# Kernel tuning notes

Hardware: AMD Instinct MI355X
Metric: run time of the kernel (lower is better)

## Reference

```python
import jax, jax.numpy as jnp
import numpy as np

D = 768
B, T = 4, 4096


def _layernorm(x, gamma, bias):
    # Faithful to the (buggy) original: (x - mu/sqrt(var)) * gamma + bias,
    # with torch's default unbiased variance (ddof=1).
    mu = jnp.mean(x, axis=-1, keepdims=True)
    var = jnp.var(x, axis=-1, keepdims=True, ddof=1)
    return (x - mu / jnp.sqrt(var)) * gamma + bias


def setup_inputs() -> dict:
    key = jax.random.key(0)
    ks = jax.random.split(key, 8)
    # kaiming_uniform_ default: bound = sqrt(6 / fan_in) with a=sqrt(5) -> gain = sqrt(2/(1+5)) = sqrt(1/3)
    # bound = gain * sqrt(3/fan_in) = sqrt(1/fan_in)
    bound_attn = 1.0 / np.sqrt(D)
    bound_lin = 1.0 / np.sqrt(D)  # torch Linear default init bound
    return {
        "x": jax.random.normal(ks[0], (B, T, D), dtype=jnp.float32),
        "ln1_g": jnp.ones((D,), jnp.float32),
        "ln1_b": jnp.zeros((D,), jnp.float32),
        "wq": jax.random.uniform(ks[1], (D, D), jnp.float32, -bound_attn, bound_attn),
        "wk": jax.random.uniform(ks[2], (D, D), jnp.float32, -bound_attn, bound_attn),
        "wv": jax.random.uniform(ks[3], (D, D), jnp.float32, -bound_attn, bound_attn),
        "ln2_g": jnp.ones((D,), jnp.float32),
        "ln2_b": jnp.zeros((D,), jnp.float32),
        "fc1_w": jax.random.uniform(ks[4], (D, D), jnp.float32, -bound_lin, bound_lin),
        "fc1_b": jax.random.uniform(ks[5], (D,), jnp.float32, -bound_lin, bound_lin),
        "fc2_w": jax.random.uniform(ks[6], (D, D), jnp.float32, -bound_lin, bound_lin),
        "fc2_b": jax.random.uniform(ks[7], (D,), jnp.float32, -bound_lin, bound_lin),
    }


def reference(x, ln1_g, ln1_b, wq, wk, wv, ln2_g, ln2_b, fc1_w, fc1_b, fc2_w, fc2_b):
    d_model = x.shape[-1]
    # LN 1
    y = _layernorm(x, ln1_g, ln1_b)
    # Naive single-head attention (no causal mask, scale 1/sqrt(d_model))
    q = jnp.einsum("btk,kd->btd", y, wq)
    k = jnp.einsum("btk,kd->btd", y, wk)
    v = jnp.einsum("btk,kd->btd", y, wv)
    scale = 1.0 / jnp.sqrt(jnp.asarray(d_model, y.dtype))
    a = jax.nn.softmax(jnp.einsum("bqd,bkd->bqk", q, k) * scale, axis=-1)
    y = jnp.einsum("bqt,btd->bqd", a, v)
    # LN 2
    y = _layernorm(y, ln2_g, ln2_b)
    # MLP: Linear -> ReLU -> Linear (Dropout in eval mode = identity)
    h = jax.nn.relu(jnp.einsum("btd,od->bto", y, fc1_w) + fc1_b)
    y = jnp.einsum("btd,od->bto", h, fc2_w) + fc2_b
    # Residual
    return x + y
```

## Files before the change

### kernel.cpp

```cpp
#include <hip/hip_runtime.h>
#include <hip/hip_bf16.h>


#define DDIM 768
#define TT   4096
#define NB   4
#define ROWS (NB * TT)

using bf16 = __hip_bfloat16;
typedef __bf16 bf16x8 __attribute__((ext_vector_type(8)));
typedef float  f32x4  __attribute__((ext_vector_type(4)));
typedef unsigned short us4 __attribute__((ext_vector_type(4)));

__device__ __forceinline__ float to_f(float x) { return x; }
__device__ __forceinline__ float to_f(bf16 x) { return __bfloat162float(x); }

__device__ __forceinline__ unsigned short bfb(float f) {
  bf16 b = __float2bfloat16(f);
  return __builtin_bit_cast(unsigned short, b);
}

__device__ __forceinline__ void gload16(const void* g, void* l) {
#if __has_builtin(__builtin_amdgcn_global_load_lds)
  __builtin_amdgcn_global_load_lds(
      (const __attribute__((address_space(1))) void*)g,
      (__attribute__((address_space(3))) void*)l, 16, 0, 0);
#else
  int lane = threadIdx.x & 63;
  ((int4*)l)[lane] = *(const int4*)g;
#endif
}

template <int MODE, int SWZ, int NT, int MT>
__global__ __launch_bounds__(256) void gemm_bt(
    const bf16* __restrict__ A, int lda, long sA,
    const bf16* __restrict__ B, int ldb, long sB,
    void* __restrict__ Cout, int ldc, long sC, int K, float scale,
    const float* __restrict__ bias, const float* __restrict__ resid,
    float* __restrict__ Lsum) {
  __shared__ __align__(16) bf16 As[128 * 32];
  __shared__ __align__(16) bf16 Bs[128 * 32];
  __shared__ float Lred[128];

  int bx, by, bz;
  if constexpr (SWZ == 1) {
    const int h   = blockIdx.x;
    const int xcd = h & 7;
    const int s   = h >> 3;
    bx = s % NT;
    const int g = (s / NT) * 8 + xcd;
    by = g % MT;
    bz = g / MT;
  } else if constexpr (SWZ == 2) {
    const int h   = blockIdx.x;
    const int xcd = h & 7;
    const int s   = h >> 3;
    by = s % MT;
    const int g = (s / MT) * 8 + xcd;
    bx = g % NT;
    bz = g / NT;
  } else {
    bx = blockIdx.x; by = blockIdx.y; bz = blockIdx.z;
  }

  A += (long)bz * sA;
  B += (long)bz * sB;

  const int tid  = threadIdx.x;
  const int wave = tid >> 6;
  const int lane = tid & 63;
  const int l16  = lane & 15;
  const int lq   = lane >> 4;
  const int wm   = wave >> 1;
  const int wn   = wave & 1;
  const long tileM = (long)by * 128;
  const long tileN = (long)bx * 128;

  if constexpr (MODE == 5) {
    if (tid < 128) Lred[tid] = 0.f;
  }

  f32x4 acc[4][4] = {};

  const int c0 = wave * 128 + lane;
  const int c1 = c0 + 64;
  bf16* ldsA0 = &As[(wave * 128 + 0) * 8];
  bf16* ldsA1 = &As[(wave * 128 + 64) * 8];
  bf16* ldsB0 = &Bs[(wave * 128 + 0) * 8];
  bf16* ldsB1 = &Bs[(wave * 128 + 64) * 8];
  const long ar0 = (tileM + (c0 >> 2)) * (long)lda + (c0 & 3) * 8;
  const long ar1 = (tileM + (c1 >> 2)) * (long)lda + (c1 & 3) * 8;
  const long br0 = (tileN + (c0 >> 2)) * (long)ldb + (c0 & 3) * 8;
  const long br1 = (tileN + (c1 >> 2)) * (long)ldb + (c1 & 3) * 8;

  for (int k0 = 0; k0 < K; k0 += 32) {
    gload16(A + ar0 + k0, ldsA0);
    gload16(A + ar1 + k0, ldsA1);
    gload16(B + br0 + k0, ldsB0);
    gload16(B + br1 + k0, ldsB1);
    __syncthreads();

    bf16x8 af[4], bf_[4];
#pragma unroll
    for (int i = 0; i < 4; ++i)
      af[i] = *(const bf16x8*)&As[(wm * 64 + i * 16 + l16) * 32 + lq * 8];
#pragma unroll
    for (int j = 0; j < 4; ++j)
      bf_[j] = *(const bf16x8*)&Bs[(wn * 64 + j * 16 + l16) * 32 + lq * 8];
#pragma unroll
    for (int i = 0; i < 4; ++i)
#pragma unroll
      for (int j = 0; j < 4; ++j)
        acc[i][j] = __builtin_amdgcn_mfma_f32_16x16x32_bf16(af[i], bf_[j],
                                                            acc[i][j], 0, 0, 0);
    __syncthreads();
  }

  const long base_m = tileM + wm * 64;
  const long base_n = tileN + wn * 64;

  if constexpr (MODE == 5) {
    bf16* P = (bf16*)Cout + (long)bz * sC;
    float ps[4] = {0.f, 0.f, 0.f, 0.f};
#pragma unroll
    for (int j = 0; j < 4; ++j) {
      const long colq = base_n + j * 16 + l16;
#pragma unroll
      for (int i = 0; i < 4; ++i) {
        const long krow = base_m + i * 16 + lq * 4;
        const float p0 = exp2f(acc[i][j][0] * scale);
        const float p1 = exp2f(acc[i][j][1] * scale);
        const float p2 = exp2f(acc[i][j][2] * scale);
        const float p3 = exp2f(acc[i][j][3] * scale);
        ps[j] += (p0 + p1) + (p2 + p3);
        us4 w = {bfb(p0), bfb(p1), bfb(p2), bfb(p3)};
        *(us4*)(P + colq * (long)ldc + krow) = w;
      }
    }
#pragma unroll
    for (int j = 0; j < 4; ++j) {
      float v = ps[j];
      v += __shfl_xor(v, 16);
      v += __shfl_xor(v, 32);
      if (lq == 0) atomicAdd(&Lred[wn * 64 + j * 16 + l16], v);
    }
    __syncthreads();
    if (tid < 128) atomicAdd(&Lsum[(long)bz * TT + tileN + tid], Lred[tid]);
  } else if constexpr (MODE == 6) {
    bf16* Op = (bf16*)Cout + (long)bz * sC;
    float inv[4];
#pragma unroll
    for (int j = 0; j < 4; ++j)
      inv[j] = 1.0f / Lsum[(long)bz * TT + base_n + j * 16 + l16];
#pragma unroll
    for (int j = 0; j < 4; ++j) {
      const long colq = base_n + j * 16 + l16;
#pragma unroll
      for (int i = 0; i < 4; ++i) {
        const long drow = base_m + i * 16 + lq * 4;
        us4 w = {bfb(acc[i][j][0] * inv[j]), bfb(acc[i][j][1] * inv[j]),
                 bfb(acc[i][j][2] * inv[j]), bfb(acc[i][j][3] * inv[j])};
        *(us4*)(Op + colq * (long)ldc + drow) = w;
      }
    }
  } else if constexpr (MODE == 3) {
    bf16* Hp = (bf16*)Cout;
#pragma unroll
    for (int i = 0; i < 4; ++i) {
      const long drow = base_m + i * 16 + lq * 4;
      const f32x4 bv = *(const f32x4*)&bias[drow];
#pragma unroll
      for (int j = 0; j < 4; ++j) {
        const long colt = base_n + j * 16 + l16;
        float v0 = acc[i][j][0] + bv[0]; v0 = v0 > 0.f ? v0 : 0.f;
        float v1 = acc[i][j][1] + bv[1]; v1 = v1 > 0.f ? v1 : 0.f;
        float v2 = acc[i][j][2] + bv[2]; v2 = v2 > 0.f ? v2 : 0.f;
        float v3 = acc[i][j][3] + bv[3]; v3 = v3 > 0.f ? v3 : 0.f;
        us4 w = {bfb(v0), bfb(v1), bfb(v2), bfb(v3)};
        *(us4*)(Hp + colt * (long)ldc + drow) = w;
      }
    }
  } else {
    float* Op = (float*)Cout;
#pragma unroll
    for (int i = 0; i < 4; ++i) {
      const long drow = base_m + i * 16 + lq * 4;
      const f32x4 bv = *(const f32x4*)&bias[drow];
#pragma unroll
      for (int j = 0; j < 4; ++j) {
        const long off = (base_n + j * 16 + l16) * (long)ldc + drow;
        const f32x4 rs = *(const f32x4*)&resid[off];
        f32x4 o;
        o[0] = acc[i][j][0] + bv[0] + rs[0];
        o[1] = acc[i][j][1] + bv[1] + rs[1];
        o[2] = acc[i][j][2] + bv[2] + rs[2];
        o[3] = acc[i][j][3] + bv[3] + rs[3];
        __builtin_nontemporal_store(o, (f32x4*)(Op + off));
      }
    }
  }
}

__global__ __launch_bounds__(256) void gemm_qkv(
    const bf16* __restrict__ Y,
    const bf16* __restrict__ Wq, const bf16* __restrict__ Wk,
    const bf16* __restrict__ Wv, bf16* __restrict__ Qm,
    bf16* __restrict__ Km, bf16* __restrict__ Vt) {
  __shared__ __align__(16) bf16 As[128 * 32];
  __shared__ __align__(16) bf16 Bs[128 * 32];

  const int z = blockIdx.z;
  const bf16* Ap = (z == 2) ? Wv : Y;
  const bf16* Bp = (z == 0) ? Wq : (z == 1) ? Wk : Y;

  const int tid  = threadIdx.x;
  const int wave = tid >> 6;
  const int lane = tid & 63;
  const int l16  = lane & 15;
  const int lq   = lane >> 4;
  const int wm   = wave >> 1;
  const int wn   = wave & 1;
  const long tileM = (z == 2) ? (long)blockIdx.x * 128 : (long)blockIdx.y * 128;
  const long tileN = (z == 2) ? (long)blockIdx.y * 128 : (long)blockIdx.x * 128;

  f32x4 acc[4][4] = {};

  const int c0 = wave * 128 + lane;
  const int c1 = c0 + 64;
  bf16* ldsA0 = &As[(wave * 128 + 0) * 8];
  bf16* ldsA1 = &As[(wave * 128 + 64) * 8];
  bf16* ldsB0 = &Bs[(wave * 128 + 0) * 8];
  bf16* ldsB1 = &Bs[(wave * 128 + 64) * 8];
  const long ar0 = (tileM + (c0 >> 2)) * (long)DDIM + (c0 & 3) * 8;
  const long ar1 = (tileM + (c1 >> 2)) * (long)DDIM + (c1 & 3) * 8;
  const long br0 = (tileN + (c0 >> 2)) * (long)DDIM + (c0 & 3) * 8;
  const long br1 = (tileN + (c1 >> 2)) * (long)DDIM + (c1 & 3) * 8;

  for (int k0 = 0; k0 < DDIM; k0 += 32) {
    gload16(Ap + ar0 + k0, ldsA0);
    gload16(Ap + ar1 + k0, ldsA1);
    gload16(Bp + br0 + k0, ldsB0);
    gload16(Bp + br1 + k0, ldsB1);
    __syncthreads();

    bf16x8 af[4], bf_[4];
#pragma unroll
    for (int i = 0; i < 4; ++i)
      af[i] = *(const bf16x8*)&As[(wm * 64 + i * 16 + l16) * 32 + lq * 8];
#pragma unroll
    for (int j = 0; j < 4; ++j)
      bf_[j] = *(const bf16x8*)&Bs[(wn * 64 + j * 16 + l16) * 32 + lq * 8];
#pragma unroll
    for (int i = 0; i < 4; ++i)
#pragma unroll
      for (int j = 0; j < 4; ++j)
        acc[i][j] = __builtin_amdgcn_mfma_f32_16x16x32_bf16(af[i], bf_[j],
                                                            acc[i][j], 0, 0, 0);
    __syncthreads();
  }

  const long base_m = tileM + wm * 64;
  const long base_n = tileN + wn * 64;
  bf16* Cp = (z == 0) ? Qm : (z == 1) ? Km : Vt;
  const long ldo = (z < 2) ? (long)DDIM : (long)ROWS;
#pragma unroll
  for (int i = 0; i < 4; ++i)
#pragma unroll
    for (int j = 0; j < 4; ++j)
#pragma unroll
      for (int r = 0; r < 4; ++r) {
        const long row = base_m + i * 16 + lq * 4 + r;
        const long col = base_n + j * 16 + l16;
        Cp[row * ldo + col] = __float2bfloat16(acc[i][j][r]);
      }
}

template <typename T>
__global__ __launch_bounds__(256) void ln_kernel(
    const T* __restrict__ in, const float* __restrict__ g,
    const float* __restrict__ beta, bf16* __restrict__ out,
    float* __restrict__ Lzero) {
  const long row = blockIdx.x;
  if (Lzero != nullptr && threadIdx.x == 0) Lzero[row] = 0.f;
  const T* xr = in + row * DDIM;
  const int t = threadIdx.x;
  float v0 = to_f(xr[t]), v1 = to_f(xr[t + 256]), v2 = to_f(xr[t + 512]);
  float s = v0 + v1 + v2;
  float q = v0 * v0 + v1 * v1 + v2 * v2;
#pragma unroll
  for (int o = 32; o; o >>= 1) {
    s += __shfl_down(s, o);
    q += __shfl_down(q, o);
  }
  __shared__ float sb[4], qb[4];
  if ((t & 63) == 0) { sb[t >> 6] = s; qb[t >> 6] = q; }
  __syncthreads();
  const float S = sb[0] + sb[1] + sb[2] + sb[3];
  const float Q = qb[0] + qb[1] + qb[2] + qb[3];
  const float mu  = S * (1.0f / 768.0f);
  const float var = (Q - 768.0f * mu * mu) * (1.0f / 767.0f);
  const float sub = mu / sqrtf(var);
  bf16* orow = out + row * DDIM;
  orow[t]       = __float2bfloat16((v0 - sub) * g[t]       + beta[t]);
  orow[t + 256] = __float2bfloat16((v1 - sub) * g[t + 256] + beta[t + 256]);
  orow[t + 512] = __float2bfloat16((v2 - sub) * g[t + 512] + beta[t + 512]);
}

__global__ void prep_weights(const float* __restrict__ wq,
                             const float* __restrict__ wk,
                             const float* __restrict__ wv,
                             const float* __restrict__ f1,
                             const float* __restrict__ f2,
                             bf16* wqt, bf16* wkt, bf16* wvt, bf16* f1b,
                             bf16* f2b) {
  __shared__ float tile[32][33];
  const float* src;
  bf16* dst;
  bool tr = true;
  switch (blockIdx.z) {
    case 0: src = wq; dst = wqt; break;
    case 1: src = wk; dst = wkt; break;
    case 2: src = wv; dst = wvt; break;
    case 3: src = f1; dst = f1b; tr = false; break;
    default: src = f2; dst = f2b; tr = false; break;
  }
  const int tx = threadIdx.x, ty = threadIdx.y;
  const int x = blockIdx.x * 32 + tx;
  const int y = blockIdx.y * 32 + ty;
  if (tr) {
#pragma unroll
    for (int r = 0; r < 4; ++r) tile[ty + 8 * r][tx] = src[(y + 8 * r) * DDIM + x];
    __syncthreads();
    const int ox = blockIdx.y * 32 + tx;
    const int oy = blockIdx.x * 32 + ty;
#pragma unroll
    for (int r = 0; r < 4; ++r)
      dst[(oy + 8 * r) * DDIM + ox] = __float2bfloat16(tile[tx][ty + 8 * r]);
  } else {
#pragma unroll
    for (int r = 0; r < 4; ++r)
      dst[(y + 8 * r) * DDIM + x] = __float2bfloat16(src[(y + 8 * r) * DDIM + x]);
  }
}

extern "C" void kernel_launch(void* const* d_in, const int* in_sizes, int n_in,
                              void* d_out, int out_size, void* d_ws,
                              size_t ws_size, hipStream_t stream) {
  const float* x     = (const float*)d_in[0];
  const float* ln1_g = (const float*)d_in[1];
  const float* ln1_b = (const float*)d_in[2];
  const float* wq    = (const float*)d_in[3];
  const float* wk    = (const float*)d_in[4];
  const float* wv    = (const float*)d_in[5];
  const float* ln2_g = (const float*)d_in[6];
  const float* ln2_b = (const float*)d_in[7];
  const float* f1w   = (const float*)d_in[8];
  const float* f1bias= (const float*)d_in[9];
  const float* f2w   = (const float*)d_in[10];
  const float* f2bias= (const float*)d_in[11];
  float* out = (float*)d_out;

  char* ws = (char*)d_ws;
  size_t off = 0;
  auto take = [&](size_t bytes) -> char* {
    char* p = ws + off;
    off += (bytes + 255) & ~(size_t)255;
    return p;
  };
  const size_t WB = (size_t)DDIM * DDIM * sizeof(bf16);
  const size_t MB = (size_t)ROWS * DDIM * sizeof(bf16);
  bf16* wqt = (bf16*)take(WB);
  bf16* wkt = (bf16*)take(WB);
  bf16* wvt = (bf16*)take(WB);
  bf16* f1b = (bf16*)take(WB);
  bf16* f2b = (bf16*)take(WB);
  float* Lsum = (float*)take((size_t)ROWS * sizeof(float));
  bf16* y1  = (bf16*)take(MB);
  bf16* Qm  = (bf16*)take(MB);
  bf16* Km  = (bf16*)take(MB);
  bf16* Vt  = (bf16*)take(MB);
  bf16* Sb  = (bf16*)take((size_t)NB * TT * TT * sizeof(bf16));
  bf16* O  = y1;
  bf16* y2 = Qm;
  bf16* h  = Km;

  prep_weights<<<dim3(24, 24, 5), dim3(32, 8), 0, stream>>>(
      wq, wk, wv, f1w, f2w, wqt, wkt, wvt, f1b, f2b);

  ln_kernel<float><<<ROWS, 256, 0, stream>>>(x, ln1_g, ln1_b, y1, Lsum);

  gemm_qkv<<<dim3(6, 128, 3), 256, 0, stream>>>(y1, wqt, wkt, wvt, Qm, Km, Vt);

  const float scale2 = 0.03608439182435161f * 1.4426950408889634f;
  gemm_bt<5, 1, 32, 32><<<dim3(32 * 32 * NB), 256, 0, stream>>>(
      Km, DDIM, (long)TT * DDIM, Qm, DDIM, (long)TT * DDIM, Sb, TT,
      (long)TT * TT, DDIM, scale2, nullptr, nullptr, Lsum);

  gemm_bt<6, 2, 32, 6><<<dim3(6 * 32 * NB), 256, 0, stream>>>(
      Vt, ROWS, (long)TT, Sb, TT, (long)TT * TT, O, DDIM, (long)TT * DDIM, TT,
      1.f, nullptr, nullptr, Lsum);

  ln_kernel<bf16><<<ROWS, 256, 0, stream>>>(O, ln2_g, ln2_b, y2, nullptr);

  gemm_bt<3, 2, 128, 6><<<dim3(128 * 6), 256, 0, stream>>>(
      f1b, DDIM, 0, y2, DDIM, 0, h, DDIM, 0, DDIM, 1.f, f1bias, nullptr,
      nullptr);
  gemm_bt<4, 2, 128, 6><<<dim3(128 * 6), 256, 0, stream>>>(
      f2b, DDIM, 0, h, DDIM, 0, out, DDIM, 0, DDIM, 1.f, f2bias, x, nullptr);
}
```

Measured before the change: 622.8 us.

## Restructure GEMMs to 2-wave blocks with K=64 tiles and XOR-swizzled LDS

All GEMM kernels now run with 128 threads (2 waves), each wave computing a 128x64 output slab (8x4 MFMA tiles) instead of 64x64 with 4 waves. The K step per LDS stage doubles from 32 to 64, halving the number of barriers. An XOR swizzle is applied to LDS placement and reads to avoid bank conflicts. This raises register pressure (32 accumulators per wave) and cuts waves per block, so occupancy and latency hiding may drop. The Lsum reduction switches from LDS atomics to direct stores.

```diff
diff --git a/kernel.cpp b/kernel.cpp
--- a/kernel.cpp
+++ b/kernel.cpp
@@ -32,14 +32,14 @@
 }
 
 template <int MODE, int SWZ, int NT, int MT>
-__global__ __launch_bounds__(256) void gemm_bt(
+__global__ __launch_bounds__(128) void gemm_bt(
     const bf16* __restrict__ A, int lda, long sA,
     const bf16* __restrict__ B, int ldb, long sB,
     void* __restrict__ Cout, int ldc, long sC, int K, float scale,
     const float* __restrict__ bias, const float* __restrict__ resid,
     float* __restrict__ Lsum) {
-  __shared__ __align__(16) bf16 As[128 * 32];
-  __shared__ __align__(16) bf16 Bs[128 * 32];
+  __shared__ __align__(16) bf16 As[128 * 64];
+  __shared__ __align__(16) bf16 Bs[128 * 64];
   __shared__ float Lred[128];
 
   int bx, by, bz;
@@ -71,52 +71,58 @@
   const int lane = tid & 63;
   const int l16  = lane & 15;
   const int lq   = lane >> 4;
-  const int wm   = wave >> 1;
-  const int wn   = wave & 1;
+  const int wn   = wave;
   const long tileM = (long)by * 128;
   const long tileN = (long)bx * 128;
 
-  if constexpr (MODE == 5) {
-    if (tid < 128) Lred[tid] = 0.f;
-  }
-
-  f32x4 acc[4][4] = {};
-
-  const int c0 = wave * 128 + lane;
-  const int c1 = c0 + 64;
-  bf16* ldsA0 = &As[(wave * 128 + 0) * 8];
-  bf16* ldsA1 = &As[(wave * 128 + 64) * 8];
-  bf16* ldsB0 = &Bs[(wave * 128 + 0) * 8];
-  bf16* ldsB1 = &Bs[(wave * 128 + 64) * 8];
-  const long ar0 = (tileM + (c0 >> 2)) * (long)lda + (c0 & 3) * 8;
-  const long ar1 = (tileM + (c1 >> 2)) * (long)lda + (c1 & 3) * 8;
-  const long br0 = (tileN + (c0 >> 2)) * (long)ldb + (c0 & 3) * 8;
-  const long br1 = (tileN + (c1 >> 2)) * (long)ldb + (c1 & 3) * 8;
-
-  for (int k0 = 0; k0 < K; k0 += 32) {
-    gload16(A + ar0 + k0, ldsA0);
-    gload16(A + ar1 + k0, ldsA1);
-    gload16(B + br0 + k0, ldsB0);
-    gload16(B + br1 + k0, ldsB1);
-    __syncthreads();
-
-    bf16x8 af[4], bf_[4];
-#pragma unroll
-    for (int i = 0; i < 4; ++i)
-      af[i] = *(const bf16x8*)&As[(wm * 64 + i * 16 + l16) * 32 + lq * 8];
-#pragma unroll
-    for (int j = 0; j < 4; ++j)
-      bf_[j] = *(const bf16x8*)&Bs[(wn * 64 + j * 16 + l16) * 32 + lq * 8];
-#pragma unroll
-    for (int i = 0; i < 4; ++i)
+  unsigned int aoff[8], boff[8];
+#pragma unroll
+  for (int q = 0; q < 8; ++q) {
+    const int p    = (q * 2 + wave) * 1024 + lane * 16;
+    const int lg   = p ^ (((p >> 7) & 7) << 4);
+    const int row  = lg >> 7;
+    const int colb = lg & 127;
+    aoff[q] = (unsigned int)((tileM + row) * (long)lda * 2 + colb);
+    boff[q] = (unsigned int)((tileN + row) * (long)ldb * 2 + colb);
+  }
+
+  f32x4 acc[8][4] = {};
+
+  const char* Ab = (const char*)A;
+  const char* Bb = (const char*)B;
+  char* AsB = (char*)As;
+  char* BsB = (char*)Bs;
+  const int sw = (l16 & 7) << 4;
+
+  for (int kb = 0; kb < K * 2; kb += 128) {
+#pragma unroll
+    for (int q = 0; q < 8; ++q)
+      gload16(Ab + (aoff[q] + kb), AsB + (q * 2 + wave) * 1024);
+#pragma unroll
+    for (int q = 0; q < 8; ++q)
+      gload16(Bb + (boff[q] + kb), BsB + (q * 2 + wave) * 1024);
+    __syncthreads();
+
+#pragma unroll
+    for (int kk = 0; kk < 2; ++kk) {
+      bf16x8 af[8], bf_[4];
+      const int ks = (kk * 64 + lq * 16) ^ sw;
+#pragma unroll
+      for (int i = 0; i < 8; ++i)
+        af[i] = *(const bf16x8*)(AsB + (i * 16 + l16) * 128 + ks);
 #pragma unroll
       for (int j = 0; j < 4; ++j)
-        acc[i][j] = __builtin_amdgcn_mfma_f32_16x16x32_bf16(af[i], bf_[j],
-                                                            acc[i][j], 0, 0, 0);
-    __syncthreads();
-  }
-
-  const long base_m = tileM + wm * 64;
+        bf_[j] = *(const bf16x8*)(BsB + (wn * 64 + j * 16 + l16) * 128 + ks);
+#pragma unroll
+      for (int i = 0; i < 8; ++i)
+#pragma unroll
+        for (int j = 0; j < 4; ++j)
+          acc[i][j] = __builtin_amdgcn_mfma_f32_16x16x32_bf16(af[i], bf_[j],
+                                                              acc[i][j], 0, 0, 0);
+    }
+    __syncthreads();
+  }
+
   const long base_n = tileN + wn * 64;
 
   if constexpr (MODE == 5) {
@@ -126,8 +132,8 @@
     for (int j = 0; j < 4; ++j) {
       const long colq = base_n + j * 16 + l16;
 #pragma unroll
-      for (int i = 0; i < 4; ++i) {
-        const long krow = base_m + i * 16 + lq * 4;
+      for (int i = 0; i < 8; ++i) {
+        const long krow = tileM + i * 16 + lq * 4;
         const float p0 = exp2f(acc[i][j][0] * scale);
         const float p1 = exp2f(acc[i][j][1] * scale);
         const float p2 = exp2f(acc[i][j][2] * scale);
@@ -142,10 +148,10 @@
       float v = ps[j];
       v += __shfl_xor(v, 16);
       v += __shfl_xor(v, 32);
-      if (lq == 0) atomicAdd(&Lred[wn * 64 + j * 16 + l16], v);
-    }
-    __syncthreads();
-    if (tid < 128) atomicAdd(&Lsum[(long)bz * TT + tileN + tid], Lred[tid]);
+      if (lq == 0) Lred[wn * 64 + j * 16 + l16] = v;
+    }
+    __syncthreads();
+    atomicAdd(&Lsum[(long)bz * TT + tileN + tid], Lred[tid]);
   } else if constexpr (MODE == 6) {
     bf16* Op = (bf16*)Cout + (long)bz * sC;
     float inv[4];
@@ -156,8 +162,8 @@
     for (int j = 0; j < 4; ++j) {
       const long colq = base_n + j * 16 + l16;
 #pragma unroll
-      for (int i = 0; i < 4; ++i) {
-        const long drow = base_m + i * 16 + lq * 4;
+      for (int i = 0; i < 8; ++i) {
+        const long drow = tileM + i * 16 + lq * 4;
         us4 w = {bfb(acc[i][j][0] * inv[j]), bfb(acc[i][j][1] * inv[j]),
                  bfb(acc[i][j][2] * inv[j]), bfb(acc[i][j][3] * inv[j])};
         *(us4*)(Op + colq * (long)ldc + drow) = w;
@@ -166,8 +172,8 @@
   } else if constexpr (MODE == 3) {
     bf16* Hp = (bf16*)Cout;
 #pragma unroll
-    for (int i = 0; i < 4; ++i) {
-      const long drow = base_m + i * 16 + lq * 4;
+    for (int i = 0; i < 8; ++i) {
+      const long drow = tileM + i * 16 + lq * 4;
       const f32x4 bv = *(const f32x4*)&bias[drow];
 #pragma unroll
       for (int j = 0; j < 4; ++j) {
@@ -183,8 +189,8 @@
   } else {
     float* Op = (float*)Cout;
 #pragma unroll
-    for (int i = 0; i < 4; ++i) {
-      const long drow = base_m + i * 16 + lq * 4;
+    for (int i = 0; i < 8; ++i) {
+      const long drow = tileM + i * 16 + lq * 4;
       const f32x4 bv = *(const f32x4*)&bias[drow];
 #pragma unroll
       for (int j = 0; j < 4; ++j) {
@@ -201,13 +207,13 @@
   }
 }
 
-__global__ __launch_bounds__(256) void gemm_qkv(
+__global__ __launch_bounds__(128) void gemm_qkv(
     const bf16* __restrict__ Y,
     const bf16* __restrict__ Wq, const bf16* __restrict__ Wk,
     const bf16* __restrict__ Wv, bf16* __restrict__ Qm,
     bf16* __restrict__ Km, bf16* __restrict__ Vt) {
-  __shared__ __align__(16) bf16 As[128 * 32];
-  __shared__ __align__(16) bf16 Bs[128 * 32];
+  __shared__ __align__(16) bf16 As[128 * 64];
+  __shared__ __align__(16) bf16 Bs[128 * 64];
 
   const int z = blockIdx.z;
   const bf16* Ap = (z == 2) ? Wv : Y;
@@ -218,58 +224,68 @@
   const int lane = tid & 63;
   const int l16  = lane & 15;
   const int lq   = lane >> 4;
-  const int wm   = wave >> 1;
-  const int wn   = wave & 1;
+  const int wn   = wave;
   const long tileM = (z == 2) ? (long)blockIdx.x * 128 : (long)blockIdx.y * 128;
   const long tileN = (z == 2) ? (long)blockIdx.y * 128 : (long)blockIdx.x * 128;
 
-  f32x4 acc[4][4] = {};
-
-  const int c0 = wave * 128 + lane;
-  const int c1 = c0 + 64;
-  bf16* ldsA0 = &As[(wave * 128 + 0) * 8];
-  bf16* ldsA1 = &As[(wave * 128 + 64) * 8];
-  bf16* ldsB0 = &Bs[(wave * 128 + 0) * 8];
-  bf16* ldsB1 = &Bs[(wave * 128 + 64) * 8];
-  const long ar0 = (tileM + (c0 >> 2)) * (long)DDIM + (c0 & 3) * 8;
-  const long ar1 = (tileM + (c1 >> 2)) * (long)DDIM + (c1 & 3) * 8;
-  const long br0 = (tileN + (c0 >> 2)) * (long)DDIM + (c0 & 3) * 8;
-  const long br1 = (tileN + (c1 >> 2)) * (long)DDIM + (c1 & 3) * 8;
-
-  for (int k0 = 0; k0 < DDIM; k0 += 32) {
-    gload16(Ap + ar0 + k0, ldsA0);
-    gload16(Ap + ar1 + k0, ldsA1);
-    gload16(Bp + br0 + k0, ldsB0);
-    gload16(Bp + br1 + k0, ldsB1);
-    __syncthreads();
-
-    bf16x8 af[4], bf_[4];
-#pragma unroll
-    for (int i = 0; i < 4; ++i)
-      af[i] = *(const bf16x8*)&As[(wm * 64 + i * 16 + l16) * 32 + lq * 8];
-#pragma unroll
-    for (int j = 0; j < 4; ++j)
-      bf_[j] = *(const bf16x8*)&Bs[(wn * 64 + j * 16 + l16) * 32 + lq * 8];
-#pragma unroll
-    for (int i = 0; i < 4; ++i)
+  unsigned int aoff[8], boff[8];
+#pragma unroll
+  for (int q = 0; q < 8; ++q) {
+    const int p    = (q * 2 + wave) * 1024 + lane * 16;
+    const int lg   = p ^ (((p >> 7) & 7) << 4);
+    const int row  = lg >> 7;
+    const int colb = lg & 127;
+    aoff[q] = (unsigned int)((tileM + row) * (long)DDIM * 2 + colb);
+    boff[q] = (unsigned int)((tileN + row) * (long)DDIM * 2 + colb);
+  }
+
+  f32x4 acc[8][4] = {};
+
+  const char* Ab = (const char*)Ap;
+  const char* Bb = (const char*)Bp;
+  char* AsB = (char*)As;
+  char* BsB = (char*)Bs;
+  const int sw = (l16 & 7) << 4;
+
+  for (int kb = 0; kb < DDIM * 2; kb += 128) {
+#pragma unroll
+    for (int q = 0; q < 8; ++q)
+      gload16(Ab + (aoff[q] + kb), AsB + (q * 2 + wave) * 1024);
+#pragma unroll
+    for (int q = 0; q < 8; ++q)
+      gload16(Bb + (boff[q] + kb), BsB + (q * 2 + wave) * 1024);
+    __syncthreads();
+
+#pragma unroll
+    for (int kk = 0; kk < 2; ++kk) {
+      bf16x8 af[8], bf_[4];
+      const int ks = (kk * 64 + lq * 16) ^ sw;
+#pragma unroll
+      for (int i = 0; i < 8; ++i)
+        af[i] = *(const bf16x8*)(AsB + (i * 16 + l16) * 128 + ks);
 #pragma unroll
       for (int j = 0; j < 4; ++j)
-        acc[i][j] = __builtin_amdgcn_mfma_f32_16x16x32_bf16(af[i], bf_[j],
-                                                            acc[i][j], 0, 0, 0);
-    __syncthreads();
-  }
-
-  const long base_m = tileM + wm * 64;
+        bf_[j] = *(const bf16x8*)(BsB + (wn * 64 + j * 16 + l16) * 128 + ks);
+#pragma unroll
+      for (int i = 0; i < 8; ++i)
+#pragma unroll
+        for (int j = 0; j < 4; ++j)
+          acc[i][j] = __builtin_amdgcn_mfma_f32_16x16x32_bf16(af[i], bf_[j],
+                                                              acc[i][j], 0, 0, 0);
+    }
+    __syncthreads();
+  }
+
   const long base_n = tileN + wn * 64;
   bf16* Cp = (z == 0) ? Qm : (z == 1) ? Km : Vt;
   const long ldo = (z < 2) ? (long)DDIM : (long)ROWS;
 #pragma unroll
-  for (int i = 0; i < 4; ++i)
+  for (int i = 0; i < 8; ++i)
 #pragma unroll
     for (int j = 0; j < 4; ++j)
 #pragma unroll
       for (int r = 0; r < 4; ++r) {
-        const long row = base_m + i * 16 + lq * 4 + r;
+        const long row = tileM + i * 16 + lq * 4 + r;
         const long col = base_n + j * 16 + l16;
         Cp[row * ldo + col] = __float2bfloat16(acc[i][j][r]);
       }
@@ -389,22 +405,22 @@
 
   ln_kernel<float><<<ROWS, 256, 0, stream>>>(x, ln1_g, ln1_b, y1, Lsum);
 
-  gemm_qkv<<<dim3(6, 128, 3), 256, 0, stream>>>(y1, wqt, wkt, wvt, Qm, Km, Vt);
+  gemm_qkv<<<dim3(6, 128, 3), 128, 0, stream>>>(y1, wqt, wkt, wvt, Qm, Km, Vt);
 
   const float scale2 = 0.03608439182435161f * 1.4426950408889634f;
-  gemm_bt<5, 1, 32, 32><<<dim3(32 * 32 * NB), 256, 0, stream>>>(
+  gemm_bt<5, 1, 32, 32><<<dim3(32 * 32 * NB), 128, 0, stream>>>(
       Km, DDIM, (long)TT * DDIM, Qm, DDIM, (long)TT * DDIM, Sb, TT,
       (long)TT * TT, DDIM, scale2, nullptr, nullptr, Lsum);
 
-  gemm_bt<6, 2, 32, 6><<<dim3(6 * 32 * NB), 256, 0, stream>>>(
+  gemm_bt<6, 2, 32, 6><<<dim3(6 * 32 * NB), 128, 0, stream>>>(
       Vt, ROWS, (long)TT, Sb, TT, (long)TT * TT, O, DDIM, (long)TT * DDIM, TT,
       1.f, nullptr, nullptr, Lsum);
 
   ln_kernel<bf16><<<ROWS, 256, 0, stream>>>(O, ln2_g, ln2_b, y2, nullptr);
 
-  gemm_bt<3, 2, 128, 6><<<dim3(128 * 6), 256, 0, stream>>>(
+  gemm_bt<3, 2, 128, 6><<<dim3(128 * 6), 128, 0, stream>>>(
       f1b, DDIM, 0, y2, DDIM, 0, h, DDIM, 0, DDIM, 1.f, f1bias, nullptr,
       nullptr);
-  gemm_bt<4, 2, 128, 6><<<dim3(128 * 6), 256, 0, stream>>>(
+  gemm_bt<4, 2, 128, 6><<<dim3(128 * 6), 128, 0, stream>>>(
       f2b, DDIM, 0, h, DDIM, 0, out, DDIM, 0, DDIM, 1.f, f2bias, x, nullptr);
 }
```

Result: slower. 756.8 us (+21.5%).
